# Kernel optimization log

Measured on AMD Instinct MI355X. Metric: run time of the kernel, lower is better.

The kernel has to match this reference:

```python
import jax, jax.numpy as jnp
import numpy as np

NUM_ITERS = 5
MIN_SCALE = 0.5
MAX_SCALE = 2.0
EPS = 1e-8


def setup_inputs() -> dict:
    key = jax.random.key(0)
    k1, k2 = jax.random.split(key)
    B, N, M = 16, 4096, 4096
    source = jax.random.normal(k1, (B, N, 3), dtype=jnp.float32)
    target = jax.random.normal(k2, (B, M, 3), dtype=jnp.float32)
    return {"source": source, "target": target}


def _sq_cdist(a, b):
    # squared euclidean distance matrix (B,N,M) via quadratic expansion
    a2 = jnp.sum(a * a, axis=-1)[:, :, None]
    b2 = jnp.sum(b * b, axis=-1)[:, None, :]
    ab = jnp.einsum('bnd,bmd->bnm', a, b)
    return jnp.maximum(a2 + b2 - 2.0 * ab, 0.0)


def _umeyama(source, target_corr):
    # optimal similarity transform (R, t, scale), Umeyama
    B = source.shape[0]
    mu_src = jnp.mean(source, axis=1, keepdims=True)       # (B,1,3)
    mu_tgt = jnp.mean(target_corr, axis=1, keepdims=True)  # (B,1,3)
    src_c = source - mu_src
    tgt_c = target_corr - mu_tgt
    H = jnp.einsum('bnd,bne->bde', src_c, tgt_c)           # (B,3,3)
    U, S, Vh = jnp.linalg.svd(H)
    V = jnp.swapaxes(Vh, 1, 2)
    det_UV = jnp.linalg.det(jnp.einsum('bij,bkj->bik', V, U))  # det(V U^T)
    d_diag = jnp.concatenate(
        [jnp.ones((B, 2), dtype=source.dtype), det_UV[:, None]], axis=1)  # (B,3)
    # R = V @ diag(d) @ U^T
    R = jnp.einsum('bij,bj,bkj->bik', V, d_diag, U)
    var_src = jnp.sum(src_c * src_c, axis=(1, 2))          # (B,)
    trace_S = jnp.sum(S * d_diag, axis=1)                  # (B,)
    scale = (trace_S / (var_src + EPS))[:, None, None]
    scale = jnp.clip(scale, MIN_SCALE, MAX_SCALE)
    t = mu_tgt - scale * jnp.einsum('bnd,bed->bne', mu_src, R)
    return R, t, scale


def reference(source, target):
    # ICP iterations (no-grad in original -> stop_gradient on final transform)
    src_current = source
    for _ in range(NUM_ITERS):
        dist = _sq_cdist(src_current, target)              # (B,N,M)
        min_idx = jnp.argmin(dist, axis=2)                 # (B,N)
        tgt_corr = jnp.take_along_axis(target, min_idx[:, :, None], axis=1)
        R, t, scale = _umeyama(source, tgt_corr)
        src_current = scale * jnp.einsum('bnd,bed->bne', source, R) + t
    R = jax.lax.stop_gradient(R)
    t = jax.lax.stop_gradient(t)
    scale = jax.lax.stop_gradient(scale)
    aligned_source = scale * jnp.einsum('bnd,bed->bne', source, R) + t
    final_dist = _sq_cdist(aligned_source, target)
    min_src2tgt = jnp.min(final_dist, axis=2)
    min_tgt2src = jnp.min(final_dist, axis=1)
    chamfer = jnp.mean(min_src2tgt, axis=1) + jnp.mean(min_tgt2src, axis=1)
    return jnp.mean(chamfer), aligned_source
```

## Files before the change

kernel.cpp:

```cpp
#include <hip/hip_runtime.h>
#include <math.h>

#define BLOCK 256
#define NB    16
#define NN_   4096
#define MM_   4096
#define NITER 5
#define P     4
#define SCH   4
#define KCH   32
#define TCH   128
#define KCHF  16
#define TCHF  256
#define SCH2  4
#define P2    4

#define OFF_STATS 0
#define OFF_T     64
#define OFF_CH    320
#define OFF_PART  336
#define OFF_ND    2048
#define OFF_FA    67584
#define OFF_FB    133120
#define CLR_BASE  2048
#define CLR_CNT   196608

typedef __attribute__((ext_vector_type(2))) float f32x2;

__device__ __forceinline__ f32x2 pk_fma(f32x2 a, f32x2 b, f32x2 c) {
  f32x2 d;
  asm("v_pk_fma_f32 %0, %1, %2, %3" : "=v"(d) : "v"(a), "v"(b), "v"(c));
  return d;
}

__device__ __forceinline__ void atomic_min_f(float* p, float v) {
  atomicMin((unsigned int*)p, __float_as_uint(v));
}

__global__ __launch_bounds__(BLOCK) void icp_init(const float* __restrict__ src,
                                                  float* __restrict__ ws) {
  int b = blockIdx.x, tid = threadIdx.x;
  for (int i = b*BLOCK + tid; i < CLR_CNT; i += NB*BLOCK)
    ws[CLR_BASE + i] = INFINITY;
  const float* sb = src + (size_t)b * NN_ * 3;
  float sx = 0.f, sy = 0.f, sz = 0.f, ss = 0.f;
  for (int n = tid; n < NN_; n += BLOCK) {
    float x = sb[3*n], y = sb[3*n+1], z = sb[3*n+2];
    sx += x; sy += y; sz += z;
    ss += fmaf(x, x, fmaf(y, y, z*z));
  }
  __shared__ float red[16];
  for (int m = 32; m; m >>= 1) {
    sx += __shfl_xor(sx, m); sy += __shfl_xor(sy, m);
    sz += __shfl_xor(sz, m); ss += __shfl_xor(ss, m);
  }
  int wave = tid >> 6;
  if ((tid & 63) == 0) {
    red[wave*4+0] = sx; red[wave*4+1] = sy; red[wave*4+2] = sz; red[wave*4+3] = ss;
  }
  __syncthreads();
  if (tid == 0) {
    for (int w = 1; w < 4; ++w) {
      sx += red[w*4+0]; sy += red[w*4+1]; sz += red[w*4+2]; ss += red[w*4+3];
    }
    float* st = ws + OFF_STATS + b*4;
    st[0] = sx; st[1] = sy; st[2] = sz; st[3] = ss;
    float* T = ws + OFF_T + b*16;
    T[0]=1.f; T[1]=0.f; T[2]=0.f;
    T[3]=0.f; T[4]=1.f; T[5]=0.f;
    T[6]=0.f; T[7]=0.f; T[8]=1.f;
    T[9]=0.f; T[10]=0.f; T[11]=0.f; T[12]=1.f;
  }
}

__global__ __launch_bounds__(BLOCK, 8) void icp_nn1(const float* __restrict__ src,
                                                    const float* __restrict__ tgt,
                                                    float* __restrict__ ws) {
  __shared__ __align__(16) float tx_[TCH], ty_[TCH], tz_[TCH], tw_[TCH];
  int b = blockIdx.z, kc = blockIdx.y, tid = threadIdx.x;
  int n0 = blockIdx.x * (BLOCK * P) + tid;
  const float* T = ws + OFF_T + b*16;
  float sc = T[12];
  f32x2 nxp[P], nyp[P], nzp[P], p2p[P];
#pragma unroll
  for (int k = 0; k < P; ++k) {
    const float* sp = src + ((size_t)b * NN_ + n0 + k*BLOCK) * 3;
    float sx = sp[0], sy = sp[1], sz = sp[2];
    float px = fmaf(sc, fmaf(T[0], sx, fmaf(T[1], sy, T[2]*sz)), T[9]);
    float py = fmaf(sc, fmaf(T[3], sx, fmaf(T[4], sy, T[5]*sz)), T[10]);
    float pz = fmaf(sc, fmaf(T[6], sx, fmaf(T[7], sy, T[8]*sz)), T[11]);
    nxp[k].x = nxp[k].y = -2.f*px;
    nyp[k].x = nyp[k].y = -2.f*py;
    nzp[k].x = nzp[k].y = -2.f*pz;
    float p2 = fmaf(px, px, fmaf(py, py, pz*pz));
    p2p[k].x = p2p[k].y = p2;
  }
  if (tid < TCH) {
    int j = tid;
    const float* tp = tgt + ((size_t)b * MM_ + kc * TCH + j) * 3;
    float tx = tp[0], ty = tp[1], tz = tp[2];
    tx_[j] = tx; ty_[j] = ty; tz_[j] = tz;
    tw_[j] = fmaf(tx, tx, fmaf(ty, ty, tz*tz));
  }
  __syncthreads();

  int jbase = kc * TCH;
  float best[P];
#pragma unroll
  for (int k = 0; k < P; ++k) best[k] = INFINITY;
#pragma unroll 4
  for (int j = 0; j < TCH; j += 2) {
    f32x2 TX = *(const f32x2*)&tx_[j];
    f32x2 TY = *(const f32x2*)&ty_[j];
    f32x2 TZ = *(const f32x2*)&tz_[j];
    f32x2 TW = *(const f32x2*)&tw_[j];
    unsigned i0 = (unsigned)(jbase + j), i1 = i0 + 1;
#pragma unroll
    for (int k = 0; k < P; ++k) {
      f32x2 v = pk_fma(nxp[k], TX, pk_fma(nyp[k], TY, pk_fma(nzp[k], TZ, TW + p2p[k])));
      float p0 = __uint_as_float((__float_as_uint(v.x) & 0xFFFFF000u) | i0);
      float p1 = __uint_as_float((__float_as_uint(v.y) & 0xFFFFF000u) | i1);
      best[k] = fminf(fminf(p0, p1), best[k]);
    }
  }
#pragma unroll
  for (int k = 0; k < P; ++k)
    atomic_min_f(ws + OFF_ND + (size_t)b*NN_ + n0 + k*BLOCK, best[k]);
}

__global__ __launch_bounds__(BLOCK) void icp_nn2(const float* __restrict__ src,
                                                 const float* __restrict__ tgt,
                                                 float* __restrict__ ws) {
  __shared__ float red[4*12];
  int b = blockIdx.y, c4 = blockIdx.x, tid = threadIdx.x;
  float acc[12];
#pragma unroll
  for (int c = 0; c < 12; ++c) acc[c] = 0.f;
  for (int k = 0; k < P2; ++k) {
    int n = c4 * (BLOCK*P2) + tid + k*BLOCK;
    size_t slot = OFF_ND + (size_t)b*NN_ + n;
    float bd = ws[slot];
    ws[slot] = INFINITY;
    int bi = (int)(__float_as_uint(bd) & 4095u);
    const float* tp = tgt + ((size_t)b * MM_ + bi) * 3;
    const float* sp = src + ((size_t)b * NN_ + n) * 3;
    float tx = tp[0], ty = tp[1], tz = tp[2];
    float sx = sp[0], sy = sp[1], sz = sp[2];
    acc[0] += tx; acc[1] += ty; acc[2] += tz;
    acc[3] += sx*tx; acc[4] += sx*ty; acc[5] += sx*tz;
    acc[6] += sy*tx; acc[7] += sy*ty; acc[8] += sy*tz;
    acc[9] += sz*tx; acc[10] += sz*ty; acc[11] += sz*tz;
  }
#pragma unroll
  for (int c = 0; c < 12; ++c)
    for (int m = 32; m; m >>= 1) acc[c] += __shfl_xor(acc[c], m);
  int wave = tid >> 6;
  if ((tid & 63) == 0) {
#pragma unroll
    for (int c = 0; c < 12; ++c) red[wave*12 + c] = acc[c];
  }
  __syncthreads();
  if (tid < 12) {
    float s = red[tid] + red[12+tid] + red[24+tid] + red[36+tid];
    ws[OFF_PART + (b*SCH2 + c4)*12 + tid] = s;
  }
}

__global__ __launch_bounds__(64) void icp_umeyama(float* __restrict__ ws) {
  int b = blockIdx.x, tid = threadIdx.x;
  __shared__ double sums[12];
  if (tid < 12) {
    double s = 0.0;
    for (int j = 0; j < SCH2; ++j)
      s += (double)ws[OFF_PART + (b*SCH2 + j)*12 + tid];
    sums[tid] = s;
  }
  __syncthreads();
  if (tid != 0) return;

  const float* st = ws + OFF_STATS + b*4;
  const double N = (double)NN_;
  double mus[3] = {st[0]/N, st[1]/N, st[2]/N};
  double var_src = (double)st[3] - N*(mus[0]*mus[0] + mus[1]*mus[1] + mus[2]*mus[2]);
  double mut[3] = {sums[0]/N, sums[1]/N, sums[2]/N};
  double H[3][3];
  for (int d = 0; d < 3; ++d)
    for (int e = 0; e < 3; ++e)
      H[d][e] = sums[3 + 3*d + e] - N*mus[d]*mut[e];

  double A[3][3];
  for (int i = 0; i < 3; ++i)
    for (int j = 0; j < 3; ++j)
      A[i][j] = H[0][i]*H[0][j] + H[1][i]*H[1][j] + H[2][i]*H[2][j];
  double V[3][3] = {{1,0,0},{0,1,0},{0,0,1}};
  const int PP[3] = {0,0,1}, QQ[3] = {1,2,2};
  for (int sweep = 0; sweep < 8; ++sweep) {
    for (int r = 0; r < 3; ++r) {
      int p = PP[r], q = QQ[r];
      double apq = A[p][q];
      if (fabs(apq) < 1e-300) continue;
      double tau = (A[q][q] - A[p][p]) / (2.0*apq);
      double tt = (tau >= 0.0 ? 1.0 : -1.0) / (fabs(tau) + sqrt(1.0 + tau*tau));
      double c = 1.0 / sqrt(1.0 + tt*tt), s = tt*c;
      for (int k = 0; k < 3; ++k) { double akp=A[k][p], akq=A[k][q];
        A[k][p]=c*akp - s*akq; A[k][q]=s*akp + c*akq; }
      for (int k = 0; k < 3; ++k) { double apk=A[p][k], aqk=A[q][k];
        A[p][k]=c*apk - s*aqk; A[q][k]=s*apk + c*aqk; }
      for (int k = 0; k < 3; ++k) { double vkp=V[k][p], vkq=V[k][q];
        V[k][p]=c*vkp - s*vkq; V[k][q]=s*vkp + c*vkq; }
    }
  }
  double lam[3] = {A[0][0], A[1][1], A[2][2]};
  int o[3] = {0,1,2};
  if (lam[o[1]] > lam[o[0]]) { int t_=o[0]; o[0]=o[1]; o[1]=t_; }
  if (lam[o[2]] > lam[o[0]]) { int t_=o[0]; o[0]=o[2]; o[2]=t_; }
  if (lam[o[2]] > lam[o[1]]) { int t_=o[1]; o[1]=o[2]; o[2]=t_; }
  double v0[3] = {V[0][o[0]], V[1][o[0]], V[2][o[0]]};
  double v1[3] = {V[0][o[1]], V[1][o[1]], V[2][o[1]]};
  double v2[3] = {V[0][o[2]], V[1][o[2]], V[2][o[2]]};

  double hv0[3], hv1[3], hv2[3];
  for (int d = 0; d < 3; ++d) {
    hv0[d] = H[d][0]*v0[0] + H[d][1]*v0[1] + H[d][2]*v0[2];
    hv1[d] = H[d][0]*v1[0] + H[d][1]*v1[1] + H[d][2]*v1[2];
    hv2[d] = H[d][0]*v2[0] + H[d][1]*v2[1] + H[d][2]*v2[2];
  }
  double S0 = sqrt(hv0[0]*hv0[0] + hv0[1]*hv0[1] + hv0[2]*hv0[2]);
  double u0[3];
  double inv0 = (S0 > 1e-30) ? 1.0/S0 : 0.0;
  u0[0]=hv0[0]*inv0; u0[1]=hv0[1]*inv0; u0[2]=hv0[2]*inv0;
  if (S0 <= 1e-30) { u0[0]=1.0; u0[1]=0.0; u0[2]=0.0; }
  double S1 = sqrt(hv1[0]*hv1[0] + hv1[1]*hv1[1] + hv1[2]*hv1[2]);
  double d01 = u0[0]*hv1[0] + u0[1]*hv1[1] + u0[2]*hv1[2];
  double w1[3] = {hv1[0]-d01*u0[0], hv1[1]-d01*u0[1], hv1[2]-d01*u0[2]};
  double n1 = sqrt(w1[0]*w1[0] + w1[1]*w1[1] + w1[2]*w1[2]);
  double u1[3];
  if (n1 > 1e-30) { u1[0]=w1[0]/n1; u1[1]=w1[1]/n1; u1[2]=w1[2]/n1; }
  else {
    double ax = fabs(u0[0]);
    double t0[3] = { ax < 0.9 ? 1.0 : 0.0, ax < 0.9 ? 0.0 : 1.0, 0.0 };
    u1[0] = u0[1]*t0[2]-u0[2]*t0[1];
    u1[1] = u0[2]*t0[0]-u0[0]*t0[2];
    u1[2] = u0[0]*t0[1]-u0[1]*t0[0];
    double nn = sqrt(u1[0]*u1[0]+u1[1]*u1[1]+u1[2]*u1[2]);
    u1[0]/=nn; u1[1]/=nn; u1[2]/=nn;
  }
  double u2[3] = {u0[1]*u1[2]-u0[2]*u1[1],
                  u0[2]*u1[0]-u0[0]*u1[2],
                  u0[0]*u1[1]-u0[1]*u1[0]};
  double s2p = u2[0]*hv2[0] + u2[1]*hv2[1] + u2[2]*hv2[2];
  double dV = v0[0]*(v1[1]*v2[2]-v1[2]*v2[1])
            - v0[1]*(v1[0]*v2[2]-v1[2]*v2[0])
            + v0[2]*(v1[0]*v2[1]-v1[1]*v2[0]);
  dV = (dV >= 0.0) ? 1.0 : -1.0;
  double traceS = S0 + S1 + dV * s2p;

  double R[3][3];
  for (int i = 0; i < 3; ++i)
    for (int k = 0; k < 3; ++k)
      R[i][k] = v0[i]*u0[k] + v1[i]*u1[k] + dV*v2[i]*u2[k];

  double scale = traceS / (var_src + 1e-8);
  scale = fmin(fmax(scale, 0.5), 2.0);
  double tv[3];
  for (int e = 0; e < 3; ++e)
    tv[e] = mut[e] - scale*(R[e][0]*mus[0] + R[e][1]*mus[1] + R[e][2]*mus[2]);

  float* T = ws + OFF_T + b*16;
  for (int e = 0; e < 3; ++e)
    for (int d = 0; d < 3; ++d)
      T[3*e + d] = (float)R[e][d];
  T[9]  = (float)tv[0]; T[10] = (float)tv[1]; T[11] = (float)tv[2];
  T[12] = (float)scale;
}

__global__ __launch_bounds__(BLOCK, 8) void icp_final(const float* __restrict__ src,
                                                      const float* __restrict__ tgt,
                                                      float* __restrict__ out,
                                                      float* __restrict__ ws) {
  __shared__ __align__(16) float tx_[TCHF], ty_[TCHF], tz_[TCHF], tw_[TCHF];
  int b = blockIdx.z, yk = blockIdx.y, tid = threadIdx.x;
  int dir = yk >> 4, kc = yk & 15;
  const float* T = ws + OFF_T + b*16;
  float sc = T[12];
  int n0 = blockIdx.x * (BLOCK * P) + tid;
  f32x2 nxp[P], nyp[P], nzp[P];
  float pp[P];

  if (dir == 0) {
#pragma unroll
    for (int k = 0; k < P; ++k) {
      const float* sp = src + ((size_t)b * NN_ + n0 + k*BLOCK) * 3;
      float sx = sp[0], sy = sp[1], sz = sp[2];
      float px = fmaf(sc, fmaf(T[0], sx, fmaf(T[1], sy, T[2]*sz)), T[9]);
      float py = fmaf(sc, fmaf(T[3], sx, fmaf(T[4], sy, T[5]*sz)), T[10]);
      float pz = fmaf(sc, fmaf(T[6], sx, fmaf(T[7], sy, T[8]*sz)), T[11]);
      if (kc == 0) {
        float* op = out + 1 + ((size_t)b * NN_ + n0 + k*BLOCK) * 3;
        op[0] = px; op[1] = py; op[2] = pz;
      }
      pp[k] = fmaf(px, px, fmaf(py, py, pz*pz));
      nxp[k].x = nxp[k].y = -2.f*px;
      nyp[k].x = nyp[k].y = -2.f*py;
      nzp[k].x = nzp[k].y = -2.f*pz;
    }
    const float* tb = tgt + ((size_t)b * MM_ + kc * TCHF) * 3;
    {
      int j = tid;
      float tx = tb[3*j], ty = tb[3*j+1], tz = tb[3*j+2];
      tx_[j] = tx; ty_[j] = ty; tz_[j] = tz;
      tw_[j] = fmaf(tx, tx, fmaf(ty, ty, tz*tz));
    }
  } else {
#pragma unroll
    for (int k = 0; k < P; ++k) {
      const float* qp = tgt + ((size_t)b * MM_ + n0 + k*BLOCK) * 3;
      float qx = qp[0], qy = qp[1], qz = qp[2];
      pp[k] = fmaf(qx, qx, fmaf(qy, qy, qz*qz));
      nxp[k].x = nxp[k].y = -2.f*qx;
      nyp[k].x = nyp[k].y = -2.f*qy;
      nzp[k].x = nzp[k].y = -2.f*qz;
    }
    const float* sb = src + ((size_t)b * NN_ + kc * TCHF) * 3;
    {
      int j = tid;
      float sx = sb[3*j], sy = sb[3*j+1], sz = sb[3*j+2];
      float ax = fmaf(sc, fmaf(T[0], sx, fmaf(T[1], sy, T[2]*sz)), T[9]);
      float ay = fmaf(sc, fmaf(T[3], sx, fmaf(T[4], sy, T[5]*sz)), T[10]);
      float az = fmaf(sc, fmaf(T[6], sx, fmaf(T[7], sy, T[8]*sz)), T[11]);
      tx_[j] = ax; ty_[j] = ay; tz_[j] = az;
      tw_[j] = fmaf(ax, ax, fmaf(ay, ay, az*az));
    }
  }
  __syncthreads();

  float best[P];
#pragma unroll
  for (int k = 0; k < P; ++k) best[k] = INFINITY;
#pragma unroll 4
  for (int j = 0; j < TCHF; j += 2) {
    f32x2 TX = *(const f32x2*)&tx_[j];
    f32x2 TY = *(const f32x2*)&ty_[j];
    f32x2 TZ = *(const f32x2*)&tz_[j];
    f32x2 TW = *(const f32x2*)&tw_[j];
#pragma unroll
    for (int k = 0; k < P; ++k) {
      f32x2 v = pk_fma(nxp[k], TX, pk_fma(nyp[k], TY, pk_fma(nzp[k], TZ, TW)));
      best[k] = fminf(fminf(v.x, v.y), best[k]);
    }
  }
  float* dst = ws + (dir ? OFF_FB : OFF_FA);
#pragma unroll
  for (int k = 0; k < P; ++k) {
    float v = fmaxf(best[k] + pp[k], 0.f);
    atomic_min_f(dst + (size_t)b*NN_ + n0 + k*BLOCK, v);
  }
}

__global__ __launch_bounds__(BLOCK) void icp_fcomb(float* __restrict__ ws) {
  __shared__ float red[4*2];
  int b = blockIdx.x, tid = threadIdx.x;
  float sa = 0.f, sb = 0.f;
  for (int g = 0; g < NN_/BLOCK; ++g) {
    int n = g*BLOCK + tid;
    sa += ws[OFF_FA + (size_t)b*NN_ + n];
    sb += ws[OFF_FB + (size_t)b*NN_ + n];
  }
  for (int m = 32; m; m >>= 1) {
    sa += __shfl_xor(sa, m); sb += __shfl_xor(sb, m);
  }
  int wave = tid >> 6;
  if ((tid & 63) == 0) { red[wave*2] = sa; red[wave*2+1] = sb; }
  __syncthreads();
  if (tid == 0) {
    sa = red[0] + red[2] + red[4] + red[6];
    sb = red[1] + red[3] + red[5] + red[7];
    ws[OFF_CH + b] = sa / (float)NN_ + sb / (float)MM_;
  }
}

__global__ __launch_bounds__(64) void icp_finalize(float* __restrict__ out,
                                                   const float* __restrict__ ws) {
  if (threadIdx.x == 0) {
    float s = 0.f;
    for (int b = 0; b < NB; ++b) s += ws[OFF_CH + b];
    out[0] = s / (float)NB;
  }
}

extern "C" void kernel_launch(void* const* d_in, const int* in_sizes, int n_in,
                              void* d_out, int out_size, void* d_ws, size_t ws_size,
                              hipStream_t stream) {
  const float* src = (const float*)d_in[0];
  const float* tgt = (const float*)d_in[1];
  float* out = (float*)d_out;
  float* ws  = (float*)d_ws;

  icp_init<<<NB, BLOCK, 0, stream>>>(src, ws);
  for (int it = 0; it < NITER; ++it) {
    icp_nn1<<<dim3(SCH, KCH, NB), BLOCK, 0, stream>>>(src, tgt, ws);
    icp_nn2<<<dim3(SCH2, NB), BLOCK, 0, stream>>>(src, tgt, ws);
    icp_umeyama<<<NB, 64, 0, stream>>>(ws);
  }
  icp_final<<<dim3(SCH, 2*KCHF, NB), BLOCK, 0, stream>>>(src, tgt, out, ws);
  icp_fcomb<<<NB, BLOCK, 0, stream>>>(ws);
  icp_finalize<<<1, 64, 0, stream>>>(out, ws);
}
```

Baseline: 322.6 us.

## Precompute SoA target/aligned-source planes and read via uniform global loads instead of LDS

Adds prep kernels that write target and final aligned-source points as SoA planes (x,y,z,|p|^2) into workspace once. The nearest-neighbour and final chamfer kernels now read these planes directly with wave-uniform 128-bit global loads instead of staging through shared memory behind a barrier. This removes per-block AoS loads, norm recomputation, the LDS round trip and the sync. It adds two extra launches and relies on the compiler turning uniform loads into scalar loads, with the cache serving repeated reads.

```diff
diff --git a/kernel.cpp b/kernel.cpp
--- a/kernel.cpp
+++ b/kernel.cpp
@@ -14,6 +14,7 @@
 #define TCHF  256
 #define SCH2  4
 #define P2    4
+#define PL    65536
 
 #define OFF_STATS 0
 #define OFF_T     64
@@ -22,10 +23,13 @@
 #define OFF_ND    2048
 #define OFF_FA    67584
 #define OFF_FB    133120
+#define OFF_TS    198656
+#define OFF_AS    460800
 #define CLR_BASE  2048
 #define CLR_CNT   196608
 
 typedef __attribute__((ext_vector_type(2))) float f32x2;
+typedef __attribute__((ext_vector_type(4))) float f32x4;
 
 __device__ __forceinline__ f32x2 pk_fma(f32x2 a, f32x2 b, f32x2 c) {
   f32x2 d;
@@ -73,13 +77,46 @@
   }
 }
 
+__global__ __launch_bounds__(BLOCK) void icp_prep_tgt(const float* __restrict__ tgt,
+                                                      float* __restrict__ tS) {
+  int b = blockIdx.y, m = blockIdx.x*BLOCK + threadIdx.x;
+  const float* tp = tgt + ((size_t)b * MM_ + m) * 3;
+  float x = tp[0], y = tp[1], z = tp[2];
+  size_t i = (size_t)b * MM_ + m;
+  tS[i]        = x;
+  tS[PL + i]   = y;
+  tS[2*PL + i] = z;
+  tS[3*PL + i] = fmaf(x, x, fmaf(y, y, z*z));
+}
+
+__global__ __launch_bounds__(BLOCK) void icp_prep_src(const float* __restrict__ src,
+                                                      const float* __restrict__ Tm,
+                                                      float* __restrict__ aS,
+                                                      float* __restrict__ out) {
+  int b = blockIdx.y, n = blockIdx.x*BLOCK + threadIdx.x;
+  const float* T = Tm + b*16;
+  float sc = T[12];
+  const float* sp = src + ((size_t)b * NN_ + n) * 3;
+  float sx = sp[0], sy = sp[1], sz = sp[2];
+  float ax = fmaf(sc, fmaf(T[0], sx, fmaf(T[1], sy, T[2]*sz)), T[9]);
+  float ay = fmaf(sc, fmaf(T[3], sx, fmaf(T[4], sy, T[5]*sz)), T[10]);
+  float az = fmaf(sc, fmaf(T[6], sx, fmaf(T[7], sy, T[8]*sz)), T[11]);
+  size_t i = (size_t)b * NN_ + n;
+  aS[i]        = ax;
+  aS[PL + i]   = ay;
+  aS[2*PL + i] = az;
+  aS[3*PL + i] = fmaf(ax, ax, fmaf(ay, ay, az*az));
+  float* op = out + 1 + i * 3;
+  op[0] = ax; op[1] = ay; op[2] = az;
+}
+
 __global__ __launch_bounds__(BLOCK, 8) void icp_nn1(const float* __restrict__ src,
-                                                    const float* __restrict__ tgt,
-                                                    float* __restrict__ ws) {
-  __shared__ __align__(16) float tx_[TCH], ty_[TCH], tz_[TCH], tw_[TCH];
+                                                    const float* __restrict__ tS,
+                                                    const float* __restrict__ Tm,
+                                                    float* __restrict__ nd) {
   int b = blockIdx.z, kc = blockIdx.y, tid = threadIdx.x;
   int n0 = blockIdx.x * (BLOCK * P) + tid;
-  const float* T = ws + OFF_T + b*16;
+  const float* T = Tm + b*16;
   float sc = T[12];
   f32x2 nxp[P], nyp[P], nzp[P], p2p[P];
 #pragma unroll
@@ -95,37 +132,40 @@
     float p2 = fmaf(px, px, fmaf(py, py, pz*pz));
     p2p[k].x = p2p[k].y = p2;
   }
-  if (tid < TCH) {
-    int j = tid;
-    const float* tp = tgt + ((size_t)b * MM_ + kc * TCH + j) * 3;
-    float tx = tp[0], ty = tp[1], tz = tp[2];
-    tx_[j] = tx; ty_[j] = ty; tz_[j] = tz;
-    tw_[j] = fmaf(tx, tx, fmaf(ty, ty, tz*tz));
-  }
-  __syncthreads();
+  const float* pX = tS + (size_t)b*MM_ + kc*TCH;
+  const float* pY = pX + PL;
+  const float* pZ = pX + 2*PL;
+  const float* pW = pX + 3*PL;
 
   int jbase = kc * TCH;
   float best[P];
 #pragma unroll
   for (int k = 0; k < P; ++k) best[k] = INFINITY;
-#pragma unroll 4
-  for (int j = 0; j < TCH; j += 2) {
-    f32x2 TX = *(const f32x2*)&tx_[j];
-    f32x2 TY = *(const f32x2*)&ty_[j];
-    f32x2 TZ = *(const f32x2*)&tz_[j];
-    f32x2 TW = *(const f32x2*)&tw_[j];
-    unsigned i0 = (unsigned)(jbase + j), i1 = i0 + 1;
+#pragma unroll 2
+  for (int j = 0; j < TCH; j += 4) {
+    f32x4 X = *(const f32x4*)&pX[j];
+    f32x4 Y = *(const f32x4*)&pY[j];
+    f32x4 Z = *(const f32x4*)&pZ[j];
+    f32x4 W = *(const f32x4*)&pW[j];
+    f32x2 X0 = {X.x, X.y}, X1 = {X.z, X.w};
+    f32x2 Y0 = {Y.x, Y.y}, Y1 = {Y.z, Y.w};
+    f32x2 Z0 = {Z.x, Z.y}, Z1 = {Z.z, Z.w};
+    f32x2 W0 = {W.x, W.y}, W1 = {W.z, W.w};
+    unsigned i0 = (unsigned)(jbase + j), i1 = i0+1, i2 = i0+2, i3 = i0+3;
 #pragma unroll
     for (int k = 0; k < P; ++k) {
-      f32x2 v = pk_fma(nxp[k], TX, pk_fma(nyp[k], TY, pk_fma(nzp[k], TZ, TW + p2p[k])));
-      float p0 = __uint_as_float((__float_as_uint(v.x) & 0xFFFFF000u) | i0);
-      float p1 = __uint_as_float((__float_as_uint(v.y) & 0xFFFFF000u) | i1);
-      best[k] = fminf(fminf(p0, p1), best[k]);
+      f32x2 v0 = pk_fma(nxp[k], X0, pk_fma(nyp[k], Y0, pk_fma(nzp[k], Z0, W0 + p2p[k])));
+      f32x2 v1 = pk_fma(nxp[k], X1, pk_fma(nyp[k], Y1, pk_fma(nzp[k], Z1, W1 + p2p[k])));
+      float q0 = __uint_as_float((__float_as_uint(v0.x) & 0xFFFFF000u) | i0);
+      float q1 = __uint_as_float((__float_as_uint(v0.y) & 0xFFFFF000u) | i1);
+      float q2 = __uint_as_float((__float_as_uint(v1.x) & 0xFFFFF000u) | i2);
+      float q3 = __uint_as_float((__float_as_uint(v1.y) & 0xFFFFF000u) | i3);
+      best[k] = fminf(fminf(fminf(q0, q1), fminf(q2, q3)), best[k]);
     }
   }
 #pragma unroll
   for (int k = 0; k < P; ++k)
-    atomic_min_f(ws + OFF_ND + (size_t)b*NN_ + n0 + k*BLOCK, best[k]);
+    atomic_min_f(nd + (size_t)b*NN_ + n0 + k*BLOCK, best[k]);
 }
 
 __global__ __launch_bounds__(BLOCK) void icp_nn2(const float* __restrict__ src,
@@ -274,82 +314,52 @@
   T[12] = (float)scale;
 }
 
-__global__ __launch_bounds__(BLOCK, 8) void icp_final(const float* __restrict__ src,
-                                                      const float* __restrict__ tgt,
-                                                      float* __restrict__ out,
-                                                      float* __restrict__ ws) {
-  __shared__ __align__(16) float tx_[TCHF], ty_[TCHF], tz_[TCHF], tw_[TCHF];
+__global__ __launch_bounds__(BLOCK, 8) void icp_final(const float* __restrict__ aS,
+                                                      const float* __restrict__ tS,
+                                                      float* __restrict__ fa,
+                                                      float* __restrict__ fb) {
   int b = blockIdx.z, yk = blockIdx.y, tid = threadIdx.x;
   int dir = yk >> 4, kc = yk & 15;
-  const float* T = ws + OFF_T + b*16;
-  float sc = T[12];
+  const float* qS = dir ? tS : aS;
+  const float* sS = dir ? aS : tS;
+  float* dst = dir ? fb : fa;
   int n0 = blockIdx.x * (BLOCK * P) + tid;
   f32x2 nxp[P], nyp[P], nzp[P];
   float pp[P];
-
-  if (dir == 0) {
+#pragma unroll
+  for (int k = 0; k < P; ++k) {
+    size_t i = (size_t)b * NN_ + n0 + k*BLOCK;
+    float qx = qS[i], qy = qS[PL + i], qz = qS[2*PL + i];
+    pp[k] = qS[3*PL + i];
+    nxp[k].x = nxp[k].y = -2.f*qx;
+    nyp[k].x = nyp[k].y = -2.f*qy;
+    nzp[k].x = nzp[k].y = -2.f*qz;
+  }
+  const float* pX = sS + (size_t)b*NN_ + kc*TCHF;
+  const float* pY = pX + PL;
+  const float* pZ = pX + 2*PL;
+  const float* pW = pX + 3*PL;
+
+  float best[P];
+#pragma unroll
+  for (int k = 0; k < P; ++k) best[k] = INFINITY;
+#pragma unroll 2
+  for (int j = 0; j < TCHF; j += 4) {
+    f32x4 X = *(const f32x4*)&pX[j];
+    f32x4 Y = *(const f32x4*)&pY[j];
+    f32x4 Z = *(const f32x4*)&pZ[j];
+    f32x4 W = *(const f32x4*)&pW[j];
+    f32x2 X0 = {X.x, X.y}, X1 = {X.z, X.w};
+    f32x2 Y0 = {Y.x, Y.y}, Y1 = {Y.z, Y.w};
+    f32x2 Z0 = {Z.x, Z.y}, Z1 = {Z.z, Z.w};
+    f32x2 W0 = {W.x, W.y}, W1 = {W.z, W.w};
 #pragma unroll
     for (int k = 0; k < P; ++k) {
-      const float* sp = src + ((size_t)b * NN_ + n0 + k*BLOCK) * 3;
-      float sx = sp[0], sy = sp[1], sz = sp[2];
-      float px = fmaf(sc, fmaf(T[0], sx, fmaf(T[1], sy, T[2]*sz)), T[9]);
-      float py = fmaf(sc, fmaf(T[3], sx, fmaf(T[4], sy, T[5]*sz)), T[10]);
-      float pz = fmaf(sc, fmaf(T[6], sx, fmaf(T[7], sy, T[8]*sz)), T[11]);
-      if (kc == 0) {
-        float* op = out + 1 + ((size_t)b * NN_ + n0 + k*BLOCK) * 3;
-        op[0] = px; op[1] = py; op[2] = pz;
-      }
-      pp[k] = fmaf(px, px, fmaf(py, py, pz*pz));
-      nxp[k].x = nxp[k].y = -2.f*px;
-      nyp[k].x = nyp[k].y = -2.f*py;
-      nzp[k].x = nzp[k].y = -2.f*pz;
+      f32x2 v0 = pk_fma(nxp[k], X0, pk_fma(nyp[k], Y0, pk_fma(nzp[k], Z0, W0)));
+      f32x2 v1 = pk_fma(nxp[k], X1, pk_fma(nyp[k], Y1, pk_fma(nzp[k], Z1, W1)));
+      best[k] = fminf(fminf(fminf(v0.x, v0.y), fminf(v1.x, v1.y)), best[k]);
     }
-    const float* tb = tgt + ((size_t)b * MM_ + kc * TCHF) * 3;
-    {
-      int j = tid;
-      float tx = tb[3*j], ty = tb[3*j+1], tz = tb[3*j+2];
-      tx_[j] = tx; ty_[j] = ty; tz_[j] = tz;
-      tw_[j] = fmaf(tx, tx, fmaf(ty, ty, tz*tz));
-    }
-  } else {
-#pragma unroll
-    for (int k = 0; k < P; ++k) {
-      const float* qp = tgt + ((size_t)b * MM_ + n0 + k*BLOCK) * 3;
-      float qx = qp[0], qy = qp[1], qz = qp[2];
-      pp[k] = fmaf(qx, qx, fmaf(qy, qy, qz*qz));
-      nxp[k].x = nxp[k].y = -2.f*qx;
-      nyp[k].x = nyp[k].y = -2.f*qy;
-      nzp[k].x = nzp[k].y = -2.f*qz;
-    }
-    const float* sb = src + ((size_t)b * NN_ + kc * TCHF) * 3;
-    {
-      int j = tid;
-      float sx = sb[3*j], sy = sb[3*j+1], sz = sb[3*j+2];
-      float ax = fmaf(sc, fmaf(T[0], sx, fmaf(T[1], sy, T[2]*sz)), T[9]);
-      float ay = fmaf(sc, fmaf(T[3], sx, fmaf(T[4], sy, T[5]*sz)), T[10]);
-      float az = fmaf(sc, fmaf(T[6], sx, fmaf(T[7], sy, T[8]*sz)), T[11]);
-      tx_[j] = ax; ty_[j] = ay; tz_[j] = az;
-      tw_[j] = fmaf(ax, ax, fmaf(ay, ay, az*az));
-    }
-  }
-  __syncthreads();
-
-  float best[P];
-#pragma unroll
-  for (int k = 0; k < P; ++k) best[k] = INFINITY;
-#pragma unroll 4
-  for (int j = 0; j < TCHF; j += 2) {
-    f32x2 TX = *(const f32x2*)&tx_[j];
-    f32x2 TY = *(const f32x2*)&ty_[j];
-    f32x2 TZ = *(const f32x2*)&tz_[j];
-    f32x2 TW = *(const f32x2*)&tw_[j];
-#pragma unroll
-    for (int k = 0; k < P; ++k) {
-      f32x2 v = pk_fma(nxp[k], TX, pk_fma(nyp[k], TY, pk_fma(nzp[k], TZ, TW)));
-      best[k] = fminf(fminf(v.x, v.y), best[k]);
-    }
-  }
-  float* dst = ws + (dir ? OFF_FB : OFF_FA);
+  }
 #pragma unroll
   for (int k = 0; k < P; ++k) {
     float v = fmaxf(best[k] + pp[k], 0.f);
@@ -397,12 +407,17 @@
   float* ws  = (float*)d_ws;
 
   icp_init<<<NB, BLOCK, 0, stream>>>(src, ws);
+  icp_prep_tgt<<<dim3(MM_/BLOCK, NB), BLOCK, 0, stream>>>(tgt, ws + OFF_TS);
   for (int it = 0; it < NITER; ++it) {
-    icp_nn1<<<dim3(SCH, KCH, NB), BLOCK, 0, stream>>>(src, tgt, ws);
+    icp_nn1<<<dim3(SCH, KCH, NB), BLOCK, 0, stream>>>(src, ws + OFF_TS,
+                                                      ws + OFF_T, ws + OFF_ND);
     icp_nn2<<<dim3(SCH2, NB), BLOCK, 0, stream>>>(src, tgt, ws);
     icp_umeyama<<<NB, 64, 0, stream>>>(ws);
   }
-  icp_final<<<dim3(SCH, 2*KCHF, NB), BLOCK, 0, stream>>>(src, tgt, out, ws);
+  icp_prep_src<<<dim3(NN_/BLOCK, NB), BLOCK, 0, stream>>>(src, ws + OFF_T,
+                                                          ws + OFF_AS, out);
+  icp_final<<<dim3(SCH, 2*KCHF, NB), BLOCK, 0, stream>>>(ws + OFF_AS, ws + OFF_TS,
+                                                         ws + OFF_FA, ws + OFF_FB);
   icp_fcomb<<<NB, BLOCK, 0, stream>>>(ws);
   icp_finalize<<<1, 64, 0, stream>>>(out, ws);
 }
```

After: 396.4 us. 1.23x slower.
